# Optimization experiments

Measured on AMD Instinct MI355X. Metric: run time of the kernel, lower is better.

The kernel has to match this reference:

```python
import jax, jax.numpy as jnp
import numpy as np

IN_F = 128
OUT_F = 128
SCALE = float(np.sqrt(OUT_F))

def swish(x):
    return x * jax.nn.sigmoid(x)

def setup_inputs() -> dict:
    key = jax.random.key(0)
    ks = jax.random.split(key, 10)
    B, A = 4, 4096
    s = 1.0 / np.sqrt(IN_F)
    return {
        "x": jax.random.normal(ks[0], (B, A, IN_F), dtype=jnp.float32),
        "connectivity": jax.random.normal(ks[1], (B, A, A), dtype=jnp.float32),
        "Wq": jax.random.uniform(ks[2], (IN_F, OUT_F), jnp.float32, -s, s),
        "Wk": jax.random.uniform(ks[3], (IN_F, OUT_F), jnp.float32, -s, s),
        "Wv": jax.random.uniform(ks[4], (IN_F, OUT_F), jnp.float32, -s, s),
        "W1": jax.random.uniform(ks[5], (OUT_F, OUT_F), jnp.float32, -s, s),
        "b1": jnp.zeros((OUT_F,), jnp.float32),
        "W2": jax.random.uniform(ks[6], (OUT_F, OUT_F), jnp.float32, -s, s),
        "b2": jnp.zeros((OUT_F,), jnp.float32),
        "gamma": jnp.ones((OUT_F,), jnp.float32),
        "beta": jnp.zeros((OUT_F,), jnp.float32),
    }

def reference(x, connectivity, Wq, Wk, Wv, W1, b1, W2, b2, gamma, beta):
    # Q,K,V projections (no bias): [B,A,D]
    Q = jnp.einsum('bah,hd->bad', x, Wq)
    K = jnp.einsum('bah,hd->bad', x, Wk)
    V = jnp.einsum('bah,hd->bad', x, Wv)
    # dense all-pairs scores with additive connectivity bias: [B,A,A]
    scores = jnp.einsum('bqd,bkd->bqk', Q, K) / SCALE + connectivity
    alpha = jax.nn.softmax(scores, axis=-1)
    # dropout p=0.0 / eval mode -> identity
    H = jnp.einsum('bqk,bkd->bqd', alpha, V)
    # Swish-MLP tail
    h = swish(H)
    h = h @ W1 + b1
    h = swish(h)
    h = h @ W2 + b2
    # LayerNorm over last dim (eps=1e-5 as torch default)
    mu = jnp.mean(h, axis=-1, keepdims=True)
    var = jnp.var(h, axis=-1, keepdims=True)
    return (h - mu) * jax.lax.rsqrt(var + 1e-5) * gamma + beta
```

## Files before the change

### kernel.cpp

```cpp
#include <hip/hip_runtime.h>

#define L2E 1.44269504088896340736f
#define INV_SCALE 0.08838834764831845f

typedef _Float16 half8 __attribute__((ext_vector_type(8)));
typedef float f32x4 __attribute__((ext_vector_type(4)));

__device__ __forceinline__ float exp2_fast(float x) {
#if __has_builtin(__builtin_amdgcn_exp2f)
  return __builtin_amdgcn_exp2f(x);
#else
  return exp2f(x);
#endif
}

__device__ __forceinline__ f32x4 mfma16(half8 a, half8 b, f32x4 c) {
  return __builtin_amdgcn_mfma_f32_16x16x32_f16(a, b, c, 0, 0, 0);
}

__device__ __forceinline__ void gload16(const void* g, void* l) {
  __builtin_amdgcn_global_load_lds(
      (const __attribute__((address_space(1))) void*)g,
      (__attribute__((address_space(3))) void*)l, 16, 0, 0);
}

__device__ __forceinline__ float swish_f(float v) {
  return v / (1.f + exp2_fast(-L2E * v));
}

__device__ __forceinline__ void stage_wt(const float* __restrict__ W,
                                         _Float16* wt, int tid) {
  const int nn = tid >> 1, hf = tid & 1;
#pragma unroll
  for (int i = 0; i < 32; ++i) {
    const int k = hf * 64 + 2 * i;
    wt[nn * 136 + k]     = (_Float16)W[k * 128 + nn];
    wt[nn * 136 + k + 1] = (_Float16)W[(k + 1) * 128 + nn];
  }
}

__global__ __launch_bounds__(256) void qkv_kernel(
    const float* __restrict__ x,
    const float* __restrict__ Wq, const float* __restrict__ Wk,
    const float* __restrict__ Wv,
    _Float16* __restrict__ Qg, _Float16* __restrict__ Kg,
    _Float16* __restrict__ Vg) {
  __shared__ __align__(16) _Float16 wt[128 * 136];
  __shared__ __align__(16) _Float16 sc[64 * 136];
  const int tid = threadIdx.x;
  const int w = tid >> 6, lane = tid & 63;
  const int n16 = lane & 15, quad = lane >> 4;
  const int blk = blockIdx.x;

  half8 xf[4];
  {
    const float* xr = x + (size_t)(blk * 64 + w * 16 + n16) * 128 + quad * 8;
#pragma unroll
    for (int kc = 0; kc < 4; ++kc) {
      float4 a = *(const float4*)(xr + kc * 32);
      float4 b = *(const float4*)(xr + kc * 32 + 4);
      half8 h;
      h[0] = (_Float16)a.x; h[1] = (_Float16)a.y;
      h[2] = (_Float16)a.z; h[3] = (_Float16)a.w;
      h[4] = (_Float16)b.x; h[5] = (_Float16)b.y;
      h[6] = (_Float16)b.z; h[7] = (_Float16)b.w;
      xf[kc] = h;
    }
  }
  const float* Ws[3] = {Wq, Wk, Wv};

  for (int mat = 0; mat < 3; ++mat) {
    stage_wt(Ws[mat], wt, tid);
    __syncthreads();
    f32x4 acc[8];
#pragma unroll
    for (int ct = 0; ct < 8; ++ct) acc[ct] = f32x4{0.f, 0.f, 0.f, 0.f};
#pragma unroll
    for (int ct = 0; ct < 8; ++ct) {
#pragma unroll
      for (int kc = 0; kc < 4; ++kc) {
        half8 wf = *(const half8*)&wt[(ct * 16 + n16) * 136 + kc * 32 + quad * 8];
        acc[ct] = mfma16(xf[kc], wf, acc[ct]);
      }
    }
#pragma unroll
    for (int ct = 0; ct < 8; ++ct)
#pragma unroll
      for (int r = 0; r < 4; ++r)
        sc[(w * 16 + quad * 4 + r) * 136 + ct * 16 + n16] = (_Float16)acc[ct][r];
    __syncthreads();

    if (mat == 0) {
#pragma unroll
      for (int i = 0; i < 4; ++i) {
        const int c = tid + 256 * i;
        const int ln = c & 63, qc = (c >> 6) & 3, rt = c >> 8;
        half8 v = *(const half8*)&sc[(rt * 16 + (ln & 15)) * 136 + qc * 32 + (ln >> 4) * 8];
        *(half8*)(Qg + ((((size_t)(blk * 4 + rt)) * 4 + qc) * 64 + ln) * 8) = v;
      }
    } else if (mat == 1) {
#pragma unroll
      for (int i = 0; i < 4; ++i) {
        const int c = tid + 256 * i;
        const int ln = c & 63, kc = (c >> 6) & 3, ct = (c >> 8) & 1, tl = (c >> 9) & 1;
        half8 v = *(const half8*)&sc[(tl * 32 + ct * 16 + (ln & 15)) * 136 + kc * 32 + (ln >> 4) * 8];
        *(half8*)(Kg + (((((size_t)(blk * 2 + tl)) * 2 + ct) * 4 + kc) * 64 + ln) * 8) = v;
      }
    } else {
#pragma unroll
      for (int i = 0; i < 4; ++i) {
        const int c = tid + 256 * i;
        const int ln = c & 63, dt = (c >> 6) & 7, tl = (c >> 9) & 1;
        const int q2 = ln >> 4, nn = ln & 15;
        half8 v;
#pragma unroll
        for (int j = 0; j < 8; ++j)
          v[j] = sc[(tl * 32 + q2 * 8 + j) * 136 + dt * 16 + nn];
        *(half8*)(Vg + ((((size_t)(blk * 2 + tl)) * 8 + dt) * 64 + ln) * 8) = v;
      }
    }
    __syncthreads();
  }
}

__global__ __launch_bounds__(256) void flash_kernel(
    const float* __restrict__ conn,
    const _Float16* __restrict__ Qg, const _Float16* __restrict__ Kg,
    const _Float16* __restrict__ Vg, _Float16* __restrict__ Hg) {
  __shared__ __align__(16) _Float16 kb0[4096], vb0[4096], kb1[4096], vb1[4096];
  __shared__ __align__(16) _Float16 pb[4][640];
  __shared__ __align__(16) _Float16 hb[4][2176];

  const int tid = threadIdx.x, w = tid >> 6, lane = tid & 63;
  const int n16 = lane & 15, quad = lane >> 4;
  const int bid = blockIdx.x;
  const int b = bid & 3, g = bid >> 2;
  const int rt_g = (b * 64 + g) * 4 + w;

  half8 qf[4];
#pragma unroll
  for (int kc = 0; kc < 4; ++kc)
    qf[kc] = *(const half8*)(Qg + (((size_t)rt_g * 4 + kc) * 64 + lane) * 8);

  f32x4 o[8];
#pragma unroll
  for (int dt = 0; dt < 8; ++dt) o[dt] = f32x4{0.f, 0.f, 0.f, 0.f};
  float m_i[4] = {-__builtin_inff(), -__builtin_inff(), -__builtin_inff(), -__builtin_inff()};
  float l_i[4] = {0.f, 0.f, 0.f, 0.f};

  const _Float16* ktile = Kg + (size_t)b * 128 * 4096;
  const _Float16* vtile = Vg + (size_t)b * 128 * 4096;
  const float* cp = conn + (size_t)b * 4096 * 4096 +
                    (size_t)(g * 64 + w * 16 + quad * 4) * 4096 + n16;
  _Float16* pw = pb[w];
  const int wbase = (tid & ~63) * 8;

  auto stage = [&](int t2, _Float16* kd, _Float16* vd) {
#pragma unroll
    for (int i = 0; i < 2; ++i) {
      gload16(ktile + (size_t)t2 * 4096 + tid * 8 + i * 2048, kd + wbase + i * 2048);
      gload16(vtile + (size_t)t2 * 4096 + tid * 8 + i * 2048, vd + wbase + i * 2048);
    }
  };
  auto ldconn = [&](int t2, float* cr) {
#pragma unroll
    for (int ct = 0; ct < 2; ++ct)
#pragma unroll
      for (int r = 0; r < 4; ++r)
        cr[ct * 4 + r] = cp[(size_t)r * 4096 + t2 * 32 + ct * 16];
  };

  float c_cur[8], c_nxt[8];
  stage(0, kb0, vb0);
  ldconn(0, c_cur);
  __syncthreads();

  auto body = [&](int t, const _Float16* kcur, const _Float16* vcur,
                  _Float16* knxt, _Float16* vnxt, float* cc, float* cn) {
    if (t + 1 < 128) {
      stage(t + 1, knxt, vnxt);
      ldconn(t + 1, cn);
    }
    f32x4 s[2];
    s[0] = f32x4{0.f, 0.f, 0.f, 0.f};
    s[1] = f32x4{0.f, 0.f, 0.f, 0.f};
#pragma unroll
    for (int ct = 0; ct < 2; ++ct)
#pragma unroll
      for (int kc = 0; kc < 4; ++kc) {
        half8 kf = *(const half8*)(kcur + ((ct * 4 + kc) * 64 + lane) * 8);
        s[ct] = mfma16(qf[kc], kf, s[ct]);
      }
    const float c1 = L2E * INV_SCALE;
    float pr[8];
#pragma unroll
    for (int ct = 0; ct < 2; ++ct)
#pragma unroll
      for (int r = 0; r < 4; ++r)
        pr[ct * 4 + r] = s[ct][r] * c1 + cc[ct * 4 + r] * L2E;
    float mt[4];
#pragma unroll
    for (int r = 0; r < 4; ++r) mt[r] = fmaxf(pr[r], pr[4 + r]);
#pragma unroll
    for (int mask = 1; mask <= 8; mask <<= 1)
#pragma unroll
      for (int r = 0; r < 4; ++r)
        mt[r] = fmaxf(mt[r], __shfl_xor(mt[r], mask, 64));
    float al[4];
#pragma unroll
    for (int r = 0; r < 4; ++r) {
      float mn = fmaxf(m_i[r], mt[r]);
      al[r] = exp2_fast(m_i[r] - mn);
      m_i[r] = mn;
    }
#pragma unroll
    for (int ct = 0; ct < 2; ++ct)
#pragma unroll
      for (int r = 0; r < 4; ++r)
        pr[ct * 4 + r] = exp2_fast(pr[ct * 4 + r] - m_i[r]);
    float rs[4];
#pragma unroll
    for (int r = 0; r < 4; ++r) rs[r] = pr[r] + pr[4 + r];
#pragma unroll
    for (int mask = 1; mask <= 8; mask <<= 1)
#pragma unroll
      for (int r = 0; r < 4; ++r) rs[r] += __shfl_xor(rs[r], mask, 64);
#pragma unroll
    for (int r = 0; r < 4; ++r) l_i[r] = l_i[r] * al[r] + rs[r];
#pragma unroll
    for (int dt = 0; dt < 8; ++dt)
#pragma unroll
      for (int r = 0; r < 4; ++r) o[dt][r] *= al[r];
#pragma unroll
    for (int ct = 0; ct < 2; ++ct)
#pragma unroll
      for (int r = 0; r < 4; ++r)
        pw[(quad * 4 + r) * 40 + ct * 16 + n16] = (_Float16)pr[ct * 4 + r];
    half8 pf = *(const half8*)(pw + n16 * 40 + quad * 8);
#pragma unroll
    for (int dt = 0; dt < 8; ++dt) {
      half8 vf = *(const half8*)(vcur + (dt * 64 + lane) * 8);
      o[dt] = mfma16(pf, vf, o[dt]);
    }
    __syncthreads();
  };

#pragma unroll 1
  for (int t = 0; t < 128; t += 2) {
    body(t, kb0, vb0, kb1, vb1, c_cur, c_nxt);
    body(t + 1, kb1, vb1, kb0, vb0, c_nxt, c_cur);
  }

  float il[4];
#pragma unroll
  for (int r = 0; r < 4; ++r) il[r] = 1.0f / l_i[r];
  _Float16* hw = hb[w];
#pragma unroll
  for (int dt = 0; dt < 8; ++dt)
#pragma unroll
    for (int r = 0; r < 4; ++r)
      hw[(quad * 4 + r) * 136 + dt * 16 + n16] = (_Float16)(o[dt][r] * il[r]);
#pragma unroll
  for (int kc = 0; kc < 4; ++kc) {
    half8 hf = *(const half8*)(hw + n16 * 136 + kc * 32 + quad * 8);
    *(half8*)(Hg + (((size_t)rt_g * 4 + kc) * 64 + lane) * 8) = hf;
  }
}

__global__ __launch_bounds__(256) void mlp_kernel(
    const _Float16* __restrict__ Hg,
    const float* __restrict__ W1, const float* __restrict__ b1,
    const float* __restrict__ W2, const float* __restrict__ b2,
    const float* __restrict__ gamma, const float* __restrict__ beta,
    float* __restrict__ out) {
  __shared__ __align__(16) _Float16 wt[128 * 136];
  __shared__ __align__(16) _Float16 hb[4][2176];
  const int tid = threadIdx.x, w = tid >> 6, lane = tid & 63;
  const int n16 = lane & 15, quad = lane >> 4;
  const int rt_g = blockIdx.x * 4 + w;

  half8 hf[4];
#pragma unroll
  for (int kc = 0; kc < 4; ++kc)
    hf[kc] = *(const half8*)(Hg + (((size_t)rt_g * 4 + kc) * 64 + lane) * 8);
#pragma unroll
  for (int kc = 0; kc < 4; ++kc)
#pragma unroll
    for (int j = 0; j < 8; ++j)
      hf[kc][j] = (_Float16)swish_f((float)hf[kc][j]);

  float b1v[8], b2v[8], gv[8], bv[8];
#pragma unroll
  for (int ct = 0; ct < 8; ++ct) {
    b1v[ct] = b1[ct * 16 + n16];
    b2v[ct] = b2[ct * 16 + n16];
    gv[ct] = gamma[ct * 16 + n16];
    bv[ct] = beta[ct * 16 + n16];
  }

  stage_wt(W1, wt, tid);
  __syncthreads();

  f32x4 acc[8];
#pragma unroll
  for (int ct = 0; ct < 8; ++ct) acc[ct] = f32x4{0.f, 0.f, 0.f, 0.f};
#pragma unroll
  for (int ct = 0; ct < 8; ++ct)
#pragma unroll
    for (int kc = 0; kc < 4; ++kc) {
      half8 wf = *(const half8*)&wt[(ct * 16 + n16) * 136 + kc * 32 + quad * 8];
      acc[ct] = mfma16(hf[kc], wf, acc[ct]);
    }
  _Float16* hw = hb[w];
#pragma unroll
  for (int ct = 0; ct < 8; ++ct)
#pragma unroll
    for (int r = 0; r < 4; ++r)
      hw[(quad * 4 + r) * 136 + ct * 16 + n16] =
          (_Float16)swish_f(acc[ct][r] + b1v[ct]);
  half8 h1f[4];
#pragma unroll
  for (int kc = 0; kc < 4; ++kc)
    h1f[kc] = *(const half8*)(hw + n16 * 136 + kc * 32 + quad * 8);
  __syncthreads();
  stage_wt(W2, wt, tid);
  __syncthreads();
#pragma unroll
  for (int ct = 0; ct < 8; ++ct) acc[ct] = f32x4{0.f, 0.f, 0.f, 0.f};
#pragma unroll
  for (int ct = 0; ct < 8; ++ct)
#pragma unroll
    for (int kc = 0; kc < 4; ++kc) {
      half8 wf = *(const half8*)&wt[(ct * 16 + n16) * 136 + kc * 32 + quad * 8];
      acc[ct] = mfma16(h1f[kc], wf, acc[ct]);
    }
  float hx[8][4];
  float sm[4] = {0, 0, 0, 0}, ss[4] = {0, 0, 0, 0};
#pragma unroll
  for (int ct = 0; ct < 8; ++ct)
#pragma unroll
    for (int r = 0; r < 4; ++r) {
      float v = acc[ct][r] + b2v[ct];
      hx[ct][r] = v;
      sm[r] += v;
      ss[r] += v * v;
    }
#pragma unroll
  for (int mask = 1; mask <= 8; mask <<= 1)
#pragma unroll
    for (int r = 0; r < 4; ++r) {
      sm[r] += __shfl_xor(sm[r], mask, 64);
      ss[r] += __shfl_xor(ss[r], mask, 64);
    }
#pragma unroll
  for (int r = 0; r < 4; ++r) {
    const float mu = sm[r] * (1.f / 128.f);
    const float var = ss[r] * (1.f / 128.f) - mu * mu;
    const float rstd = rsqrtf(var + 1e-5f);
    const size_t row = (size_t)rt_g * 16 + quad * 4 + r;
#pragma unroll
    for (int ct = 0; ct < 8; ++ct)
      out[row * 128 + ct * 16 + n16] = (hx[ct][r] - mu) * rstd * gv[ct] + bv[ct];
  }
}

extern "C" void kernel_launch(void* const* d_in, const int* in_sizes, int n_in,
                              void* d_out, int out_size, void* d_ws,
                              size_t ws_size, hipStream_t stream) {
  const float* x     = (const float*)d_in[0];
  const float* conn  = (const float*)d_in[1];
  const float* Wq    = (const float*)d_in[2];
  const float* Wk    = (const float*)d_in[3];
  const float* Wv    = (const float*)d_in[4];
  const float* W1    = (const float*)d_in[5];
  const float* b1    = (const float*)d_in[6];
  const float* W2    = (const float*)d_in[7];
  const float* b2    = (const float*)d_in[8];
  const float* gamma = (const float*)d_in[9];
  const float* beta  = (const float*)d_in[10];
  float* out = (float*)d_out;

  const size_t N = (size_t)16384 * 128;
  _Float16* Qg = (_Float16*)d_ws;
  _Float16* Kg = Qg + N;
  _Float16* Vg = Kg + N;
  _Float16* Hg = Vg + N;

  qkv_kernel<<<256, 256, 0, stream>>>(x, Wq, Wk, Wv, Qg, Kg, Vg);
  flash_kernel<<<256, 256, 0, stream>>>(conn, Qg, Kg, Vg, Hg);
  mlp_kernel<<<256, 256, 0, stream>>>(Hg, W1, b1, W2, b2, gamma, beta, out);
}
```

Baseline: 487.8 us.

## Split flash attention over key range, pre-pack weights, fuse Q projection into attention

Adds a prep kernel that converts all five weight matrices to fp16 in MFMA fragment order once, so the other kernels read fragments straight from global memory instead of transposing into LDS. Q is now computed inside the flash kernel, which uses 128-thread blocks and an optional 2-way split along the key axis (split-K). Partial outputs are saved with their running max and sum, and the MLP kernel merges them. Other changes: DPP-based row reductions, lazy rescaling that runs only when the max grows, and connectivity pre-multiplied by log2(e). These raise occupancy and grid parallelism for the bandwidth-bound connectivity stream, at the cost of extra workspace, an extra launch and a merge step.

```diff
diff --git a/kernel.cpp b/kernel.cpp
--- a/kernel.cpp
+++ b/kernel.cpp
@@ -28,24 +28,47 @@
   return v / (1.f + exp2_fast(-L2E * v));
 }
 
-__device__ __forceinline__ void stage_wt(const float* __restrict__ W,
-                                         _Float16* wt, int tid) {
-  const int nn = tid >> 1, hf = tid & 1;
-#pragma unroll
-  for (int i = 0; i < 32; ++i) {
-    const int k = hf * 64 + 2 * i;
-    wt[nn * 136 + k]     = (_Float16)W[k * 128 + nn];
-    wt[nn * 136 + k + 1] = (_Float16)W[(k + 1) * 128 + nn];
-  }
-}
-
-__global__ __launch_bounds__(256) void qkv_kernel(
-    const float* __restrict__ x,
+template <int CTRL>
+__device__ __forceinline__ float dppmov(float x) {
+  int xi = __builtin_bit_cast(int, x);
+  int r = __builtin_amdgcn_update_dpp(xi, xi, CTRL, 0xf, 0xf, false);
+  return __builtin_bit_cast(float, r);
+}
+__device__ __forceinline__ float red16_max(float x) {
+  x = fmaxf(x, dppmov<0xB1>(x));
+  x = fmaxf(x, dppmov<0x4E>(x));
+  x = fmaxf(x, dppmov<0x141>(x));
+  x = fmaxf(x, dppmov<0x140>(x));
+  return x;
+}
+__device__ __forceinline__ float red16_sum(float x) {
+  x += dppmov<0xB1>(x);
+  x += dppmov<0x4E>(x);
+  x += dppmov<0x141>(x);
+  x += dppmov<0x140>(x);
+  return x;
+}
+
+__global__ __launch_bounds__(256) void prep_kernel(
     const float* __restrict__ Wq, const float* __restrict__ Wk,
-    const float* __restrict__ Wv,
-    _Float16* __restrict__ Qg, _Float16* __restrict__ Kg,
-    _Float16* __restrict__ Vg) {
-  __shared__ __align__(16) _Float16 wt[128 * 136];
+    const float* __restrict__ Wv, const float* __restrict__ W1,
+    const float* __restrict__ W2, _Float16* __restrict__ Wf) {
+  const int g = blockIdx.x * 256 + threadIdx.x;
+  const int mat = g >> 11, rem = g & 2047;
+  const int f = rem >> 6, lane = rem & 63;
+  const int n = (f >> 2) * 16 + (lane & 15);
+  const int k0 = (f & 3) * 32 + (lane >> 4) * 8;
+  const float* W = (mat == 0) ? Wq : (mat == 1) ? Wk : (mat == 2) ? Wv
+                   : (mat == 3) ? W1 : W2;
+  half8 h;
+#pragma unroll
+  for (int j = 0; j < 8; ++j) h[j] = (_Float16)W[(k0 + j) * 128 + n];
+  *(half8*)(Wf + (size_t)g * 8) = h;
+}
+
+__global__ __launch_bounds__(256) void kv_kernel(
+    const float* __restrict__ x, const _Float16* __restrict__ Wf,
+    _Float16* __restrict__ Kg, _Float16* __restrict__ Vg) {
   __shared__ __align__(16) _Float16 sc[64 * 136];
   const int tid = threadIdx.x;
   const int w = tid >> 6, lane = tid & 63;
@@ -67,22 +90,19 @@
       xf[kc] = h;
     }
   }
-  const float* Ws[3] = {Wq, Wk, Wv};
-
-  for (int mat = 0; mat < 3; ++mat) {
-    stage_wt(Ws[mat], wt, tid);
-    __syncthreads();
+
+  for (int mat = 0; mat < 2; ++mat) {
     f32x4 acc[8];
 #pragma unroll
     for (int ct = 0; ct < 8; ++ct) acc[ct] = f32x4{0.f, 0.f, 0.f, 0.f};
 #pragma unroll
-    for (int ct = 0; ct < 8; ++ct) {
+    for (int ct = 0; ct < 8; ++ct)
 #pragma unroll
       for (int kc = 0; kc < 4; ++kc) {
-        half8 wf = *(const half8*)&wt[(ct * 16 + n16) * 136 + kc * 32 + quad * 8];
+        half8 wf = *(const half8*)(Wf +
+            ((size_t)((mat + 1) * 32 + ct * 4 + kc) * 64 + lane) * 8);
         acc[ct] = mfma16(xf[kc], wf, acc[ct]);
       }
-    }
 #pragma unroll
     for (int ct = 0; ct < 8; ++ct)
 #pragma unroll
@@ -94,17 +114,10 @@
 #pragma unroll
       for (int i = 0; i < 4; ++i) {
         const int c = tid + 256 * i;
-        const int ln = c & 63, qc = (c >> 6) & 3, rt = c >> 8;
-        half8 v = *(const half8*)&sc[(rt * 16 + (ln & 15)) * 136 + qc * 32 + (ln >> 4) * 8];
-        *(half8*)(Qg + ((((size_t)(blk * 4 + rt)) * 4 + qc) * 64 + ln) * 8) = v;
-      }
-    } else if (mat == 1) {
-#pragma unroll
-      for (int i = 0; i < 4; ++i) {
-        const int c = tid + 256 * i;
         const int ln = c & 63, kc = (c >> 6) & 3, ct = (c >> 8) & 1, tl = (c >> 9) & 1;
-        half8 v = *(const half8*)&sc[(tl * 32 + ct * 16 + (ln & 15)) * 136 + kc * 32 + (ln >> 4) * 8];
-        *(half8*)(Kg + (((((size_t)(blk * 2 + tl)) * 2 + ct) * 4 + kc) * 64 + ln) * 8) = v;
+        half8 v = *(const half8*)&sc[(tl * 32 + ct * 16 + (ln & 15)) * 136 +
+                                     kc * 32 + (ln >> 4) * 8];
+        *(half8*)(Kg + ((((size_t)(blk * 2 + tl)) * 2 + ct) * 4 + kc) * 512 + ln * 8) = v;
       }
     } else {
 #pragma unroll
@@ -116,178 +129,222 @@
 #pragma unroll
         for (int j = 0; j < 8; ++j)
           v[j] = sc[(tl * 32 + q2 * 8 + j) * 136 + dt * 16 + nn];
-        *(half8*)(Vg + ((((size_t)(blk * 2 + tl)) * 8 + dt) * 64 + ln) * 8) = v;
+        *(half8*)(Vg + (((size_t)(blk * 2 + tl)) * 8 + dt) * 512 + ln * 8) = v;
       }
     }
     __syncthreads();
   }
 }
 
-__global__ __launch_bounds__(256) void flash_kernel(
-    const float* __restrict__ conn,
-    const _Float16* __restrict__ Qg, const _Float16* __restrict__ Kg,
-    const _Float16* __restrict__ Vg, _Float16* __restrict__ Hg) {
-  __shared__ __align__(16) _Float16 kb0[4096], vb0[4096], kb1[4096], vb1[4096];
-  __shared__ __align__(16) _Float16 pb[4][640];
-  __shared__ __align__(16) _Float16 hb[4][2176];
+__global__ __launch_bounds__(128) void flash_kernel(
+    const float* __restrict__ x, const float* __restrict__ conn,
+    const _Float16* __restrict__ Wf,
+    const _Float16* __restrict__ Kg, const _Float16* __restrict__ Vg,
+    _Float16* __restrict__ Og, float2* __restrict__ Ml,
+    int nsplit, int nt) {
+  __shared__ __align__(16) _Float16 kb[2][4096];
+  __shared__ __align__(16) _Float16 vb[2][4096];
+  __shared__ __align__(16) _Float16 pb[2][656];
 
   const int tid = threadIdx.x, w = tid >> 6, lane = tid & 63;
   const int n16 = lane & 15, quad = lane >> 4;
   const int bid = blockIdx.x;
-  const int b = bid & 3, g = bid >> 2;
-  const int rt_g = (b * 64 + g) * 4 + w;
+  const int sk = bid & (nsplit - 1);
+  const int rest = (nsplit == 2) ? (bid >> 1) : bid;
+  const int batch = rest & 3;
+  const int rg = rest >> 2;
+  const int rt_g = batch * 256 + rg * 2 + w;
+  const int t0 = sk * nt;
 
   half8 qf[4];
-#pragma unroll
-  for (int kc = 0; kc < 4; ++kc)
-    qf[kc] = *(const half8*)(Qg + (((size_t)rt_g * 4 + kc) * 64 + lane) * 8);
+  {
+    half8 xf[4];
+    const float* xr = x + (size_t)(batch * 4096 + rg * 32 + w * 16 + n16) * 128 + quad * 8;
+#pragma unroll
+    for (int kc = 0; kc < 4; ++kc) {
+      float4 a = *(const float4*)(xr + kc * 32);
+      float4 b = *(const float4*)(xr + kc * 32 + 4);
+      half8 h;
+      h[0] = (_Float16)a.x; h[1] = (_Float16)a.y;
+      h[2] = (_Float16)a.z; h[3] = (_Float16)a.w;
+      h[4] = (_Float16)b.x; h[5] = (_Float16)b.y;
+      h[6] = (_Float16)b.z; h[7] = (_Float16)b.w;
+      xf[kc] = h;
+    }
+    _Float16* tw = &kb[w][0];
+#pragma unroll
+    for (int ct = 0; ct < 8; ++ct) {
+      f32x4 aq = f32x4{0.f, 0.f, 0.f, 0.f};
+#pragma unroll
+      for (int kc = 0; kc < 4; ++kc) {
+        half8 wf = *(const half8*)(Wf + ((size_t)(ct * 4 + kc) * 64 + lane) * 8);
+        aq = mfma16(xf[kc], wf, aq);
+      }
+#pragma unroll
+      for (int r = 0; r < 4; ++r)
+        tw[(quad * 4 + r) * 136 + ct * 16 + n16] = (_Float16)aq[r];
+    }
+#pragma unroll
+    for (int kc = 0; kc < 4; ++kc)
+      qf[kc] = *(const half8*)(tw + n16 * 136 + kc * 32 + quad * 8);
+  }
+  __syncthreads();
+
+  const _Float16* Kt = Kg + (size_t)batch * 524288;
+  const _Float16* Vt = Vg + (size_t)batch * 524288;
+  const float* cp = conn + (size_t)batch * 16777216 +
+                    (size_t)(rg * 32 + w * 16 + quad * 4) * 4096 + n16 +
+                    (size_t)t0 * 32;
+  const int wbase = (tid & ~63) * 8;
+
+  auto stage = [&](int t, int buf) {
+    const _Float16* ks = Kt + (size_t)t * 4096 + tid * 8;
+    const _Float16* vs = Vt + (size_t)t * 4096 + tid * 8;
+#pragma unroll
+    for (int c = 0; c < 4; ++c) {
+      gload16(ks + c * 1024, &kb[buf][c * 1024 + wbase]);
+      gload16(vs + c * 1024, &vb[buf][c * 1024 + wbase]);
+    }
+  };
+  float cc[8], cn[8];
+  auto ldconn = [&](int i, float* cr) {
+    const float* c0 = cp + (size_t)i * 32;
+#pragma unroll
+    for (int ct = 0; ct < 2; ++ct)
+#pragma unroll
+      for (int r = 0; r < 4; ++r)
+        cr[ct * 4 + r] = c0[(size_t)r * 4096 + ct * 16] * L2E;
+  };
 
   f32x4 o[8];
 #pragma unroll
   for (int dt = 0; dt < 8; ++dt) o[dt] = f32x4{0.f, 0.f, 0.f, 0.f};
-  float m_i[4] = {-__builtin_inff(), -__builtin_inff(), -__builtin_inff(), -__builtin_inff()};
+  float m_i[4] = {-__builtin_inff(), -__builtin_inff(),
+                  -__builtin_inff(), -__builtin_inff()};
   float l_i[4] = {0.f, 0.f, 0.f, 0.f};
 
-  const _Float16* ktile = Kg + (size_t)b * 128 * 4096;
-  const _Float16* vtile = Vg + (size_t)b * 128 * 4096;
-  const float* cp = conn + (size_t)b * 4096 * 4096 +
-                    (size_t)(g * 64 + w * 16 + quad * 4) * 4096 + n16;
-  _Float16* pw = pb[w];
-  const int wbase = (tid & ~63) * 8;
-
-  auto stage = [&](int t2, _Float16* kd, _Float16* vd) {
-#pragma unroll
-    for (int i = 0; i < 2; ++i) {
-      gload16(ktile + (size_t)t2 * 4096 + tid * 8 + i * 2048, kd + wbase + i * 2048);
-      gload16(vtile + (size_t)t2 * 4096 + tid * 8 + i * 2048, vd + wbase + i * 2048);
-    }
-  };
-  auto ldconn = [&](int t2, float* cr) {
-#pragma unroll
-    for (int ct = 0; ct < 2; ++ct)
-#pragma unroll
-      for (int r = 0; r < 4; ++r)
-        cr[ct * 4 + r] = cp[(size_t)r * 4096 + t2 * 32 + ct * 16];
-  };
-
-  float c_cur[8], c_nxt[8];
-  stage(0, kb0, vb0);
-  ldconn(0, c_cur);
+  stage(t0, 0);
+  ldconn(0, cc);
   __syncthreads();
 
-  auto body = [&](int t, const _Float16* kcur, const _Float16* vcur,
-                  _Float16* knxt, _Float16* vnxt, float* cc, float* cn) {
-    if (t + 1 < 128) {
-      stage(t + 1, knxt, vnxt);
-      ldconn(t + 1, cn);
-    }
-    f32x4 s[2];
-    s[0] = f32x4{0.f, 0.f, 0.f, 0.f};
-    s[1] = f32x4{0.f, 0.f, 0.f, 0.f};
-#pragma unroll
-    for (int ct = 0; ct < 2; ++ct)
-#pragma unroll
-      for (int kc = 0; kc < 4; ++kc) {
-        half8 kf = *(const half8*)(kcur + ((ct * 4 + kc) * 64 + lane) * 8);
-        s[ct] = mfma16(qf[kc], kf, s[ct]);
-      }
+#pragma unroll 1
+  for (int i = 0; i < nt; ++i) {
+    const int cur = i & 1, nxt = cur ^ 1;
+    if (i + 1 < nt) {
+      stage(t0 + i + 1, nxt);
+      ldconn(i + 1, cn);
+    }
+    f32x4 s0 = f32x4{0.f, 0.f, 0.f, 0.f};
+    f32x4 s1 = f32x4{0.f, 0.f, 0.f, 0.f};
+#pragma unroll
+    for (int kc = 0; kc < 4; ++kc) {
+      half8 kf0 = *(const half8*)&kb[cur][(0 * 4 + kc) * 512 + lane * 8];
+      half8 kf1 = *(const half8*)&kb[cur][(1 * 4 + kc) * 512 + lane * 8];
+      s0 = mfma16(qf[kc], kf0, s0);
+      s1 = mfma16(qf[kc], kf1, s1);
+    }
     const float c1 = L2E * INV_SCALE;
     float pr[8];
 #pragma unroll
-    for (int ct = 0; ct < 2; ++ct)
-#pragma unroll
-      for (int r = 0; r < 4; ++r)
-        pr[ct * 4 + r] = s[ct][r] * c1 + cc[ct * 4 + r] * L2E;
+    for (int r = 0; r < 4; ++r) pr[r] = fmaf(s0[r], c1, cc[r]);
+#pragma unroll
+    for (int r = 0; r < 4; ++r) pr[4 + r] = fmaf(s1[r], c1, cc[4 + r]);
     float mt[4];
 #pragma unroll
-    for (int r = 0; r < 4; ++r) mt[r] = fmaxf(pr[r], pr[4 + r]);
-#pragma unroll
-    for (int mask = 1; mask <= 8; mask <<= 1)
-#pragma unroll
-      for (int r = 0; r < 4; ++r)
-        mt[r] = fmaxf(mt[r], __shfl_xor(mt[r], mask, 64));
-    float al[4];
-#pragma unroll
-    for (int r = 0; r < 4; ++r) {
-      float mn = fmaxf(m_i[r], mt[r]);
-      al[r] = exp2_fast(m_i[r] - mn);
-      m_i[r] = mn;
-    }
-#pragma unroll
-    for (int ct = 0; ct < 2; ++ct)
-#pragma unroll
-      for (int r = 0; r < 4; ++r)
-        pr[ct * 4 + r] = exp2_fast(pr[ct * 4 + r] - m_i[r]);
-    float rs[4];
-#pragma unroll
-    for (int r = 0; r < 4; ++r) rs[r] = pr[r] + pr[4 + r];
-#pragma unroll
-    for (int mask = 1; mask <= 8; mask <<= 1)
-#pragma unroll
-      for (int r = 0; r < 4; ++r) rs[r] += __shfl_xor(rs[r], mask, 64);
-#pragma unroll
-    for (int r = 0; r < 4; ++r) l_i[r] = l_i[r] * al[r] + rs[r];
-#pragma unroll
-    for (int dt = 0; dt < 8; ++dt)
-#pragma unroll
-      for (int r = 0; r < 4; ++r) o[dt][r] *= al[r];
-#pragma unroll
-    for (int ct = 0; ct < 2; ++ct)
-#pragma unroll
-      for (int r = 0; r < 4; ++r)
-        pw[(quad * 4 + r) * 40 + ct * 16 + n16] = (_Float16)pr[ct * 4 + r];
+    for (int r = 0; r < 4; ++r) mt[r] = red16_max(fmaxf(pr[r], pr[4 + r]));
+    int upd = (mt[0] > m_i[0]) | (mt[1] > m_i[1]) |
+              (mt[2] > m_i[2]) | (mt[3] > m_i[3]);
+    if (__any(upd)) {
+#pragma unroll
+      for (int r = 0; r < 4; ++r) {
+        const float mn = fmaxf(m_i[r], mt[r]);
+        const float al = exp2_fast(m_i[r] - mn);
+        m_i[r] = mn;
+        l_i[r] *= al;
+#pragma unroll
+        for (int dt = 0; dt < 8; ++dt) o[dt][r] *= al;
+      }
+    }
+#pragma unroll
+    for (int c = 0; c < 8; ++c) pr[c] = exp2_fast(pr[c] - m_i[c & 3]);
+#pragma unroll
+    for (int r = 0; r < 4; ++r) l_i[r] += red16_sum(pr[r] + pr[4 + r]);
+    _Float16* pw = pb[w];
+#pragma unroll
+    for (int c = 0; c < 8; ++c)
+      pw[(quad * 4 + (c & 3)) * 40 + (c >> 2) * 16 + n16] = (_Float16)pr[c];
     half8 pf = *(const half8*)(pw + n16 * 40 + quad * 8);
 #pragma unroll
     for (int dt = 0; dt < 8; ++dt) {
-      half8 vf = *(const half8*)(vcur + (dt * 64 + lane) * 8);
+      half8 vf = *(const half8*)&vb[cur][dt * 512 + lane * 8];
       o[dt] = mfma16(pf, vf, o[dt]);
     }
+#pragma unroll
+    for (int c = 0; c < 8; ++c) cc[c] = cn[c];
     __syncthreads();
-  };
-
-#pragma unroll 1
-  for (int t = 0; t < 128; t += 2) {
-    body(t, kb0, vb0, kb1, vb1, c_cur, c_nxt);
-    body(t + 1, kb1, vb1, kb0, vb0, c_nxt, c_cur);
   }
 
   float il[4];
 #pragma unroll
-  for (int r = 0; r < 4; ++r) il[r] = 1.0f / l_i[r];
-  _Float16* hw = hb[w];
+  for (int r = 0; r < 4; ++r) il[r] = 1.f / l_i[r];
+  _Float16* tw = &kb[w][0];
 #pragma unroll
   for (int dt = 0; dt < 8; ++dt)
 #pragma unroll
     for (int r = 0; r < 4; ++r)
-      hw[(quad * 4 + r) * 136 + dt * 16 + n16] = (_Float16)(o[dt][r] * il[r]);
+      tw[(quad * 4 + r) * 136 + dt * 16 + n16] = (_Float16)(o[dt][r] * il[r]);
+  _Float16* ob = Og + ((size_t)(sk * 1024 + rt_g) * 4) * 512;
 #pragma unroll
   for (int kc = 0; kc < 4; ++kc) {
-    half8 hf = *(const half8*)(hw + n16 * 136 + kc * 32 + quad * 8);
-    *(half8*)(Hg + (((size_t)rt_g * 4 + kc) * 64 + lane) * 8) = hf;
+    half8 of = *(const half8*)(tw + n16 * 136 + kc * 32 + quad * 8);
+    *(half8*)(ob + kc * 512 + lane * 8) = of;
+  }
+  if (n16 == 0) {
+#pragma unroll
+    for (int r = 0; r < 4; ++r)
+      Ml[sk * 16384 + rt_g * 16 + quad * 4 + r] = make_float2(m_i[r], l_i[r]);
   }
 }
 
 __global__ __launch_bounds__(256) void mlp_kernel(
-    const _Float16* __restrict__ Hg,
-    const float* __restrict__ W1, const float* __restrict__ b1,
-    const float* __restrict__ W2, const float* __restrict__ b2,
+    const _Float16* __restrict__ Og, const float2* __restrict__ Ml,
+    const _Float16* __restrict__ Wf,
+    const float* __restrict__ b1, const float* __restrict__ b2,
     const float* __restrict__ gamma, const float* __restrict__ beta,
-    float* __restrict__ out) {
-  __shared__ __align__(16) _Float16 wt[128 * 136];
+    float* __restrict__ out, int nsplit) {
   __shared__ __align__(16) _Float16 hb[4][2176];
   const int tid = threadIdx.x, w = tid >> 6, lane = tid & 63;
   const int n16 = lane & 15, quad = lane >> 4;
   const int rt_g = blockIdx.x * 4 + w;
 
+  float2 ml[2];
+  float m = -__builtin_inff();
+  for (int s = 0; s < nsplit; ++s) {
+    ml[s] = Ml[s * 16384 + rt_g * 16 + n16];
+    m = fmaxf(m, ml[s].x);
+  }
+  float wgt[2], wsum = 0.f;
+  for (int s = 0; s < nsplit; ++s) {
+    wgt[s] = ml[s].y * exp2_fast(ml[s].x - m);
+    wsum += wgt[s];
+  }
+  const float inv = 1.f / wsum;
+
   half8 hf[4];
 #pragma unroll
-  for (int kc = 0; kc < 4; ++kc)
-    hf[kc] = *(const half8*)(Hg + (((size_t)rt_g * 4 + kc) * 64 + lane) * 8);
-#pragma unroll
-  for (int kc = 0; kc < 4; ++kc)
-#pragma unroll
-    for (int j = 0; j < 8; ++j)
-      hf[kc][j] = (_Float16)swish_f((float)hf[kc][j]);
+  for (int kc = 0; kc < 4; ++kc) {
+    float hv[8] = {0, 0, 0, 0, 0, 0, 0, 0};
+    for (int s = 0; s < nsplit; ++s) {
+      half8 ofr = *(const half8*)(Og +
+          ((size_t)(s * 1024 + rt_g) * 4 + kc) * 512 + lane * 8);
+#pragma unroll
+      for (int j = 0; j < 8; ++j) hv[j] += wgt[s] * (float)ofr[j];
+    }
+    half8 h;
+#pragma unroll
+    for (int j = 0; j < 8; ++j) h[j] = (_Float16)swish_f(hv[j] * inv);
+    hf[kc] = h;
+  }
 
   float b1v[8], b2v[8], gv[8], bv[8];
 #pragma unroll
@@ -298,9 +355,6 @@
     bv[ct] = beta[ct * 16 + n16];
   }
 
-  stage_wt(W1, wt, tid);
-  __syncthreads();
-
   f32x4 acc[8];
 #pragma unroll
   for (int ct = 0; ct < 8; ++ct) acc[ct] = f32x4{0.f, 0.f, 0.f, 0.f};
@@ -308,7 +362,8 @@
   for (int ct = 0; ct < 8; ++ct)
 #pragma unroll
     for (int kc = 0; kc < 4; ++kc) {
-      half8 wf = *(const half8*)&wt[(ct * 16 + n16) * 136 + kc * 32 + quad * 8];
+      half8 wf = *(const half8*)(Wf +
+          ((size_t)(3 * 32 + ct * 4 + kc) * 64 + lane) * 8);
       acc[ct] = mfma16(hf[kc], wf, acc[ct]);
     }
   _Float16* hw = hb[w];
@@ -322,16 +377,15 @@
 #pragma unroll
   for (int kc = 0; kc < 4; ++kc)
     h1f[kc] = *(const half8*)(hw + n16 * 136 + kc * 32 + quad * 8);
-  __syncthreads();
-  stage_wt(W2, wt, tid);
-  __syncthreads();
+
 #pragma unroll
   for (int ct = 0; ct < 8; ++ct) acc[ct] = f32x4{0.f, 0.f, 0.f, 0.f};
 #pragma unroll
   for (int ct = 0; ct < 8; ++ct)
 #pragma unroll
     for (int kc = 0; kc < 4; ++kc) {
-      half8 wf = *(const half8*)&wt[(ct * 16 + n16) * 136 + kc * 32 + quad * 8];
+      half8 wf = *(const half8*)(Wf +
+          ((size_t)(4 * 32 + ct * 4 + kc) * 64 + lane) * 8);
       acc[ct] = mfma16(h1f[kc], wf, acc[ct]);
     }
   float hx[8][4];
@@ -340,18 +394,16 @@
   for (int ct = 0; ct < 8; ++ct)
 #pragma unroll
     for (int r = 0; r < 4; ++r) {
-      float v = acc[ct][r] + b2v[ct];
+      const float v = acc[ct][r] + b2v[ct];
       hx[ct][r] = v;
       sm[r] += v;
       ss[r] += v * v;
     }
 #pragma unroll
-  for (int mask = 1; mask <= 8; mask <<= 1)
-#pragma unroll
-    for (int r = 0; r < 4; ++r) {
-      sm[r] += __shfl_xor(sm[r], mask, 64);
-      ss[r] += __shfl_xor(ss[r], mask, 64);
-    }
+  for (int r = 0; r < 4; ++r) {
+    sm[r] = red16_sum(sm[r]);
+    ss[r] = red16_sum(ss[r]);
+  }
 #pragma unroll
   for (int r = 0; r < 4; ++r) {
     const float mu = sm[r] * (1.f / 128.f);
@@ -380,13 +432,21 @@
   const float* beta  = (const float*)d_in[10];
   float* out = (float*)d_out;
 
-  const size_t N = (size_t)16384 * 128;
-  _Float16* Qg = (_Float16*)d_ws;
-  _Float16* Kg = Qg + N;
-  _Float16* Vg = Kg + N;
-  _Float16* Hg = Vg + N;
-
-  qkv_kernel<<<256, 256, 0, stream>>>(x, Wq, Wk, Wv, Qg, Kg, Vg);
-  flash_kernel<<<256, 256, 0, stream>>>(conn, Qg, Kg, Vg, Hg);
-  mlp_kernel<<<256, 256, 0, stream>>>(Hg, W1, b1, W2, b2, gamma, beta, out);
-}
+  const size_t need2 =
+      ((size_t)81920 + 4 * 2097152) * 2 + 2 * 16384 * sizeof(float2);
+  const int nsplit = (ws_size >= need2) ? 2 : 1;
+  const int nt = 128 / nsplit;
+
+  _Float16* Wf = (_Float16*)d_ws;
+  _Float16* Kg = Wf + 81920;
+  _Float16* Vg = Kg + 2097152;
+  _Float16* Og = Vg + 2097152;
+  float2* Ml = (float2*)(Og + (size_t)2097152 * nsplit);
+
+  prep_kernel<<<40, 256, 0, stream>>>(Wq, Wk, Wv, W1, W2, Wf);
+  kv_kernel<<<256, 256, 0, stream>>>(x, Wf, Kg, Vg);
+  flash_kernel<<<512 * nsplit, 128, 0, stream>>>(x, conn, Wf, Kg, Vg, Og, Ml,
+                                                 nsplit, nt);
+  mlp_kernel<<<256, 256, 0, stream>>>(Og, Ml, Wf, b1, b2, gamma, beta, out,
+                                      nsplit);
+}
```

New measurement: 470.1 us. 1.04x faster.
